# Performance work log

Hardware: AMD Instinct MI355X
Metric: run time of the kernel (lower is better)

Reference implementation:

```python
import jax, jax.numpy as jnp
import numpy as np

B, SQ, SK, D = 8, 4096, 4096, 64


def setup_inputs() -> dict:
    key = jax.random.key(0)
    k1, k2, k3 = jax.random.split(key, 3)
    x1 = jax.random.normal(k1, (B, SQ, D), dtype=jnp.float32)   # queries
    x2 = jax.random.normal(k2, (B, SK, D), dtype=jnp.float32)   # keys
    x3 = jax.random.normal(k3, (B, SK, D), dtype=jnp.float32)   # values
    x4 = 0                                                      # dropout p (static, 0 => deterministic)
    x5 = jnp.ones((1,), dtype=jnp.float32)                      # scale divisor
    return {"x1": x1, "x2": x2, "x3": x3, "x4": x4, "x5": x5}


def reference(x1, x2, x3, x4, x5):
    # scores: [B, Sq, Sk]
    scores = jnp.einsum("bqd,bkd->bqk", x1, x2) / x5
    attn = jax.nn.softmax(scores, axis=-1)
    p = float(x4)  # static python scalar
    if p > 0.0:
        mask = jax.random.bernoulli(jax.random.key(42), 1.0 - p, attn.shape)
        attn = attn * mask.astype(attn.dtype) / (1.0 - p)
    # out: [B, Sq, D]
    return jnp.einsum("bqk,bkd->bqd", attn, x3)
```

## Files before the change

kernel.cpp:

```cpp
#include <hip/hip_runtime.h>


typedef _Float16 f16x8 __attribute__((ext_vector_type(8)));
typedef _Float16 f16x4 __attribute__((ext_vector_type(4)));
typedef __fp16   h16x2 __attribute__((ext_vector_type(2)));
typedef float    f32x4 __attribute__((ext_vector_type(4)));

constexpr int kB  = 8;
constexpr int kSQ = 4096;
constexpr int kSK = 4096;
constexpr int kD  = 64;
constexpr int KSPLIT = 2;
constexpr int SKH = kSK / KSPLIT;
constexpr int BQ  = 128;
constexpr int BK  = 64;
constexpr int LDK = kD + 8;
constexpr int LDV = BK + 8;
constexpr int LDP = BK + 8;
constexpr size_t APART = (size_t)kB * kSQ * kD;

static __device__ __forceinline__ f16x4 pack4(float a, float b, float c, float d) {
    h16x2 p0 = __builtin_amdgcn_cvt_pkrtz(a, b);
    h16x2 p1 = __builtin_amdgcn_cvt_pkrtz(c, d);
    f16x4 r;
    r[0] = (_Float16)p0[0]; r[1] = (_Float16)p0[1];
    r[2] = (_Float16)p1[0]; r[3] = (_Float16)p1[1];
    return r;
}

__global__ __launch_bounds__(256, 2)
void fattn_partial(const float* __restrict__ Qg,
                   const float* __restrict__ Kg,
                   const float* __restrict__ Vg,
                   const float* __restrict__ sdiv,
                   float* __restrict__ Ap,
                   float2* __restrict__ MLp)
{
    __shared__ __align__(16) _Float16 sK[2][BK][LDK];
    __shared__ __align__(16) _Float16 sV[2][kD][LDV];
    __shared__ __align__(16) _Float16 sP[4][2][16][LDP];

    const int tid  = threadIdx.x;
    const int w    = tid >> 6;
    const int lane = tid & 63;
    const int l16  = lane & 15;
    const int quad = lane >> 4;

    const int b  = blockIdx.y;
    const int qb = blockIdx.x * BQ;
    const int ks = blockIdx.z;

    const float inv_scale = 1.0f / sdiv[0];

    const float* Qb = Qg + ((size_t)b * kSQ + qb) * kD;
    const float* Kb = Kg + ((size_t)b * kSK + (size_t)ks * SKH) * kD;
    const float* Vb = Vg + ((size_t)b * kSK + (size_t)ks * SKH) * kD;

    f16x8 qf[2][2];
#pragma unroll
    for (int mt = 0; mt < 2; ++mt) {
        const float* qrow = Qb + (size_t)(w * 32 + mt * 16 + l16) * kD;
#pragma unroll
        for (int kk = 0; kk < 2; ++kk) {
            const float4 a = *(const float4*)(qrow + kk * 32 + quad * 8);
            const float4 c = *(const float4*)(qrow + kk * 32 + quad * 8 + 4);
            f16x4 lo = pack4(a.x * inv_scale, a.y * inv_scale, a.z * inv_scale, a.w * inv_scale);
            f16x4 hi = pack4(c.x * inv_scale, c.y * inv_scale, c.z * inv_scale, c.w * inv_scale);
            f16x8 f;
            f[0] = lo[0]; f[1] = lo[1]; f[2] = lo[2]; f[3] = lo[3];
            f[4] = hi[0]; f[5] = hi[1]; f[6] = hi[2]; f[7] = hi[3];
            qf[mt][kk] = f;
        }
    }

    const int kp0 = 2 * ((0 * 256 + tid) >> 4), cb0 = ((0 * 256 + tid) & 15) * 4;
    const int kp1 = 2 * ((1 * 256 + tid) >> 4), cb1 = ((1 * 256 + tid) & 15) * 4;
    const int kq  = tid >> 4;
    const int fq  = tid & 15;
    const int kqs = (kq ^ (fq & 14)) * 4;

    float4 rk[2][2];
    float4 rv[4];

    auto load_tile = [&](int kt) {
        const float* Kt = Kb + (size_t)kt * BK * kD;
        const float* Vt = Vb + (size_t)kt * BK * kD;
        rk[0][0] = *(const float4*)(Kt + (kp0 + 0) * kD + cb0);
        rk[0][1] = *(const float4*)(Kt + (kp0 + 1) * kD + cb0);
        rk[1][0] = *(const float4*)(Kt + (kp1 + 0) * kD + cb1);
        rk[1][1] = *(const float4*)(Kt + (kp1 + 1) * kD + cb1);
#pragma unroll
        for (int r = 0; r < 4; ++r)
            rv[r] = *(const float4*)(Vt + (4 * kq + r) * kD + 4 * fq);
    };

    auto write_tile = [&](int buf) {
        *(f16x4*)&sK[buf][kp0 + 0][cb0] = pack4(rk[0][0].x, rk[0][0].y, rk[0][0].z, rk[0][0].w);
        *(f16x4*)&sK[buf][kp0 + 1][cb0] = pack4(rk[0][1].x, rk[0][1].y, rk[0][1].z, rk[0][1].w);
        *(f16x4*)&sK[buf][kp1 + 0][cb1] = pack4(rk[1][0].x, rk[1][0].y, rk[1][0].z, rk[1][0].w);
        *(f16x4*)&sK[buf][kp1 + 1][cb1] = pack4(rk[1][1].x, rk[1][1].y, rk[1][1].z, rk[1][1].w);
        const float vx[4][4] = {
            {rv[0].x, rv[0].y, rv[0].z, rv[0].w},
            {rv[1].x, rv[1].y, rv[1].z, rv[1].w},
            {rv[2].x, rv[2].y, rv[2].z, rv[2].w},
            {rv[3].x, rv[3].y, rv[3].z, rv[3].w}};
#pragma unroll
        for (int j = 0; j < 4; ++j)
            *(f16x4*)&sV[buf][4 * fq + j][kqs] =
                pack4(vx[0][j], vx[1][j], vx[2][j], vx[3][j]);
    };

    f32x4 o[2][4];
    float m_i[2] = {-1e30f, -1e30f}, l_i[2] = {0.0f, 0.0f};
#pragma unroll
    for (int mt = 0; mt < 2; ++mt)
#pragma unroll
        for (int dt = 0; dt < 4; ++dt)
#pragma unroll
            for (int r = 0; r < 4; ++r) o[mt][dt][r] = 0.0f;

    load_tile(0);
    write_tile(0);
    __syncthreads();

    const int nIter = SKH / BK;
    for (int kt = 0; kt < nIter; ++kt) {
        const int buf = kt & 1;
        const bool more = (kt + 1 < nIter);
        if (more) load_tile(kt + 1);

        f32x4 s[2][4];
#pragma unroll
        for (int nt = 0; nt < 4; ++nt) {
            const f16x8 kf0 = *(const f16x8*)&sK[buf][nt * 16 + l16][quad * 8];
            const f16x8 kf1 = *(const f16x8*)&sK[buf][nt * 16 + l16][32 + quad * 8];
#pragma unroll
            for (int mt = 0; mt < 2; ++mt) {
                f32x4 acc;
#pragma unroll
                for (int r = 0; r < 4; ++r) acc[r] = 0.0f;
                acc = __builtin_amdgcn_mfma_f32_16x16x32_f16(kf0, qf[mt][0], acc, 0, 0, 0);
                acc = __builtin_amdgcn_mfma_f32_16x16x32_f16(kf1, qf[mt][1], acc, 0, 0, 0);
                s[mt][nt] = acc;
            }
        }

#pragma unroll
        for (int mt = 0; mt < 2; ++mt) {
            float rm = s[mt][0][0];
#pragma unroll
            for (int nt = 0; nt < 4; ++nt)
#pragma unroll
                for (int r = 0; r < 4; ++r) rm = fmaxf(rm, s[mt][nt][r]);
            rm = fmaxf(rm, __shfl_xor(rm, 16, 64));
            rm = fmaxf(rm, __shfl_xor(rm, 32, 64));
            const float mnew = fmaxf(m_i[mt], rm);
            const float alpha = __expf(m_i[mt] - mnew);
            m_i[mt] = mnew;
            float rs = 0.0f;
#pragma unroll
            for (int nt = 0; nt < 4; ++nt)
#pragma unroll
                for (int r = 0; r < 4; ++r) {
                    const float p = __expf(s[mt][nt][r] - mnew);
                    s[mt][nt][r] = p;
                    rs += p;
                }
            rs += __shfl_xor(rs, 16, 64);
            rs += __shfl_xor(rs, 32, 64);
            l_i[mt] = l_i[mt] * alpha + rs;
#pragma unroll
            for (int dt = 0; dt < 4; ++dt)
#pragma unroll
                for (int r = 0; r < 4; ++r) o[mt][dt][r] *= alpha;
#pragma unroll
            for (int nt = 0; nt < 4; ++nt)
                *(f16x4*)&sP[w][mt][l16][nt * 16 + quad * 4] =
                    pack4(s[mt][nt][0], s[mt][nt][1], s[mt][nt][2], s[mt][nt][3]);
        }

        const f16x8 pfa0 = *(const f16x8*)&sP[w][0][l16][quad * 8];
        const f16x8 pfa1 = *(const f16x8*)&sP[w][0][l16][32 + quad * 8];
        const f16x8 pfb0 = *(const f16x8*)&sP[w][1][l16][quad * 8];
        const f16x8 pfb1 = *(const f16x8*)&sP[w][1][l16][32 + quad * 8];
#pragma unroll
        for (int dt = 0; dt < 4; ++dt) {
            const int f  = dt * 16 + l16;
            const int sw = (f >> 2) & 14;
            const f16x8 vf0 = *(const f16x8*)&sV[buf][f][((2 * quad) ^ sw) * 4];
            const f16x8 vf1 = *(const f16x8*)&sV[buf][f][((8 + 2 * quad) ^ sw) * 4];
            o[0][dt] = __builtin_amdgcn_mfma_f32_16x16x32_f16(vf0, pfa0, o[0][dt], 0, 0, 0);
            o[0][dt] = __builtin_amdgcn_mfma_f32_16x16x32_f16(vf1, pfa1, o[0][dt], 0, 0, 0);
            o[1][dt] = __builtin_amdgcn_mfma_f32_16x16x32_f16(vf0, pfb0, o[1][dt], 0, 0, 0);
            o[1][dt] = __builtin_amdgcn_mfma_f32_16x16x32_f16(vf1, pfb1, o[1][dt], 0, 0, 0);
        }

        if (more) write_tile(buf ^ 1);
        __syncthreads();
    }

    float* Ab = Ap + (size_t)ks * APART + ((size_t)b * kSQ + qb) * kD;
    float2* MLb = MLp + (size_t)ks * kB * kSQ + (size_t)b * kSQ + qb;
#pragma unroll
    for (int mt = 0; mt < 2; ++mt) {
        const int row = w * 32 + mt * 16 + l16;
#pragma unroll
        for (int dt = 0; dt < 4; ++dt) {
            float4 st4;
            st4.x = o[mt][dt][0];
            st4.y = o[mt][dt][1];
            st4.z = o[mt][dt][2];
            st4.w = o[mt][dt][3];
            *(float4*)&Ab[(size_t)row * kD + dt * 16 + quad * 4] = st4;
        }
        if (quad == 0) MLb[row] = make_float2(m_i[mt], l_i[mt]);
    }
}

__global__ __launch_bounds__(256)
void fattn_combine(const float* __restrict__ Ap,
                   const float2* __restrict__ MLp,
                   float* __restrict__ Og)
{
    const int idx = blockIdx.x * 256 + threadIdx.x;
    const int r = idx >> 4;
    const int c = (idx & 15) * 4;

    const float2 ml0 = MLp[r];
    const float2 ml1 = MLp[kB * kSQ + r];
    const float m = fmaxf(ml0.x, ml1.x);
    const float e0 = __expf(ml0.x - m);
    const float e1 = __expf(ml1.x - m);
    const float inv = 1.0f / (e0 * ml0.y + e1 * ml1.y);

    const float4 a0 = *(const float4*)&Ap[(size_t)r * kD + c];
    const float4 a1 = *(const float4*)&Ap[APART + (size_t)r * kD + c];
    float4 res;
    res.x = (e0 * a0.x + e1 * a1.x) * inv;
    res.y = (e0 * a0.y + e1 * a1.y) * inv;
    res.z = (e0 * a0.z + e1 * a1.z) * inv;
    res.w = (e0 * a0.w + e1 * a1.w) * inv;
    *(float4*)&Og[(size_t)r * kD + c] = res;
}

extern "C" void kernel_launch(void* const* d_in, const int* in_sizes, int n_in,
                              void* d_out, int out_size, void* d_ws, size_t ws_size,
                              hipStream_t stream) {
    const float* Q    = (const float*)d_in[0];
    const float* K    = (const float*)d_in[1];
    const float* V    = (const float*)d_in[2];
    const float* sdiv = (const float*)d_in[4];
    float* O = (float*)d_out;

    float*  Ap  = (float*)d_ws;
    float2* MLp = (float2*)(Ap + KSPLIT * APART);

    dim3 grid(kSQ / BQ, kB, KSPLIT);
    fattn_partial<<<grid, dim3(256), 0, stream>>>(Q, K, V, sdiv, Ap, MLp);
    fattn_combine<<<dim3(kB * kSQ * kD / (256 * 4)), dim3(256), 0, stream>>>(Ap, MLp, O);
}
```

Measured before the change: 153.9 us.

## Pre-convert K/V to swizzled fp16 and stream tiles directly into LDS

After: 146.7 us. 1.05x faster.

```diff
diff --git a/kernel.cpp b/kernel.cpp
--- a/kernel.cpp
+++ b/kernel.cpp
@@ -10,12 +10,10 @@
 constexpr int kSQ = 4096;
 constexpr int kSK = 4096;
 constexpr int kD  = 64;
-constexpr int KSPLIT = 2;
+constexpr int KSPLIT = 4;
 constexpr int SKH = kSK / KSPLIT;
 constexpr int BQ  = 128;
 constexpr int BK  = 64;
-constexpr int LDK = kD + 8;
-constexpr int LDV = BK + 8;
 constexpr int LDP = BK + 8;
 constexpr size_t APART = (size_t)kB * kSQ * kD;
 
@@ -27,17 +25,84 @@
     r[2] = (_Float16)p1[0]; r[3] = (_Float16)p1[1];
     return r;
 }
+static __device__ __forceinline__ f16x8 pack8(const float4& a, const float4& c) {
+    f16x4 lo = pack4(a.x, a.y, a.z, a.w);
+    f16x4 hi = pack4(c.x, c.y, c.z, c.w);
+    f16x8 f;
+    f[0] = lo[0]; f[1] = lo[1]; f[2] = lo[2]; f[3] = lo[3];
+    f[4] = hi[0]; f[5] = hi[1]; f[6] = hi[2]; f[7] = hi[3];
+    return f;
+}
+
+typedef const __attribute__((address_space(1))) unsigned int* gu32p;
+typedef __attribute__((address_space(3))) unsigned int* lu32p;
+static __device__ __forceinline__ void gload_lds16(const void* g, void* l) {
+    __builtin_amdgcn_global_load_lds((gu32p)g, (lu32p)l, 16, 0, 0);
+}
 
 __global__ __launch_bounds__(256, 2)
+void fattn_prepass(const float* __restrict__ Kg,
+                   const float* __restrict__ Vg,
+                   _Float16* __restrict__ Kh,
+                   _Float16* __restrict__ Vt)
+{
+    __shared__ _Float16 tr[kD][BK];
+
+    const int tid = threadIdx.x;
+    const int kt  = blockIdx.x;
+    const int b   = blockIdx.y;
+
+    const int k = tid >> 2;
+    const int p = tid & 3;
+    const int gk = kt * BK + k;
+
+    {
+        const float* src = Kg + ((size_t)b * kSK + gk) * kD + p * 16;
+        const float4 a0 = *(const float4*)(src + 0);
+        const float4 a1 = *(const float4*)(src + 4);
+        const float4 a2 = *(const float4*)(src + 8);
+        const float4 a3 = *(const float4*)(src + 12);
+        _Float16* dst = Kh + ((size_t)b * kSK + gk) * kD;
+        const int fb0 = 2 * p, fb1 = 2 * p + 1;
+        *(f16x8*)&dst[(fb0 ^ (gk & 7)) * 8] = pack8(a0, a1);
+        *(f16x8*)&dst[(fb1 ^ (gk & 7)) * 8] = pack8(a2, a3);
+    }
+
+    {
+        const float* src = Vg + ((size_t)b * kSK + gk) * kD + p * 16;
+        const float4 a0 = *(const float4*)(src + 0);
+        const float4 a1 = *(const float4*)(src + 4);
+        const float4 a2 = *(const float4*)(src + 8);
+        const float4 a3 = *(const float4*)(src + 12);
+        const float v[16] = {a0.x,a0.y,a0.z,a0.w, a1.x,a1.y,a1.z,a1.w,
+                             a2.x,a2.y,a2.z,a2.w, a3.x,a3.y,a3.z,a3.w};
+#pragma unroll
+        for (int j = 0; j < 16; ++j)
+            tr[p * 16 + j][k] = (_Float16)v[j];
+    }
+    __syncthreads();
+    {
+        const int f  = tid >> 2;
+        const int p2 = tid & 3;
+        const f16x8 b0 = *(const f16x8*)&tr[f][p2 * 16 + 0];
+        const f16x8 b1 = *(const f16x8*)&tr[f][p2 * 16 + 8];
+        _Float16* dst = Vt + (((size_t)b * 64 + kt) * kD + f) * BK;
+        const int kb0 = 2 * p2, kb1 = 2 * p2 + 1;
+        *(f16x8*)&dst[(kb0 ^ (f & 7)) * 8] = b0;
+        *(f16x8*)&dst[(kb1 ^ (f & 7)) * 8] = b1;
+    }
+}
+
+__global__ __launch_bounds__(256, 3)
 void fattn_partial(const float* __restrict__ Qg,
-                   const float* __restrict__ Kg,
-                   const float* __restrict__ Vg,
+                   const _Float16* __restrict__ Kh,
+                   const _Float16* __restrict__ Vt,
                    const float* __restrict__ sdiv,
-                   float* __restrict__ Ap,
+                   _Float16* __restrict__ Ap,
                    float2* __restrict__ MLp)
 {
-    __shared__ __align__(16) _Float16 sK[2][BK][LDK];
-    __shared__ __align__(16) _Float16 sV[2][kD][LDV];
+    __shared__ __align__(16) _Float16 sK[2][BK * kD];
+    __shared__ __align__(16) _Float16 sV[2][kD * BK];
     __shared__ __align__(16) _Float16 sP[4][2][16][LDP];
 
     const int tid  = threadIdx.x;
@@ -45,6 +110,7 @@
     const int lane = tid & 63;
     const int l16  = lane & 15;
     const int quad = lane >> 4;
+    const int sw   = (quad ^ (l16 & 7)) * 8;
 
     const int b  = blockIdx.y;
     const int qb = blockIdx.x * BQ;
@@ -53,8 +119,8 @@
     const float inv_scale = 1.0f / sdiv[0];
 
     const float* Qb = Qg + ((size_t)b * kSQ + qb) * kD;
-    const float* Kb = Kg + ((size_t)b * kSK + (size_t)ks * SKH) * kD;
-    const float* Vb = Vg + ((size_t)b * kSK + (size_t)ks * SKH) * kD;
+    const _Float16* Khb = Kh + ((size_t)b * kSK + (size_t)ks * SKH) * kD;
+    const _Float16* Vtb = Vt + (((size_t)b * 64 + (size_t)ks * (SKH / BK)) * kD) * BK;
 
     f16x8 qf[2][2];
 #pragma unroll
@@ -64,50 +130,21 @@
         for (int kk = 0; kk < 2; ++kk) {
             const float4 a = *(const float4*)(qrow + kk * 32 + quad * 8);
             const float4 c = *(const float4*)(qrow + kk * 32 + quad * 8 + 4);
-            f16x4 lo = pack4(a.x * inv_scale, a.y * inv_scale, a.z * inv_scale, a.w * inv_scale);
-            f16x4 hi = pack4(c.x * inv_scale, c.y * inv_scale, c.z * inv_scale, c.w * inv_scale);
-            f16x8 f;
-            f[0] = lo[0]; f[1] = lo[1]; f[2] = lo[2]; f[3] = lo[3];
-            f[4] = hi[0]; f[5] = hi[1]; f[6] = hi[2]; f[7] = hi[3];
-            qf[mt][kk] = f;
-        }
-    }
-
-    const int kp0 = 2 * ((0 * 256 + tid) >> 4), cb0 = ((0 * 256 + tid) & 15) * 4;
-    const int kp1 = 2 * ((1 * 256 + tid) >> 4), cb1 = ((1 * 256 + tid) & 15) * 4;
-    const int kq  = tid >> 4;
-    const int fq  = tid & 15;
-    const int kqs = (kq ^ (fq & 14)) * 4;
-
-    float4 rk[2][2];
-    float4 rv[4];
-
-    auto load_tile = [&](int kt) {
-        const float* Kt = Kb + (size_t)kt * BK * kD;
-        const float* Vt = Vb + (size_t)kt * BK * kD;
-        rk[0][0] = *(const float4*)(Kt + (kp0 + 0) * kD + cb0);
-        rk[0][1] = *(const float4*)(Kt + (kp0 + 1) * kD + cb0);
-        rk[1][0] = *(const float4*)(Kt + (kp1 + 0) * kD + cb1);
-        rk[1][1] = *(const float4*)(Kt + (kp1 + 1) * kD + cb1);
-#pragma unroll
-        for (int r = 0; r < 4; ++r)
-            rv[r] = *(const float4*)(Vt + (4 * kq + r) * kD + 4 * fq);
-    };
-
-    auto write_tile = [&](int buf) {
-        *(f16x4*)&sK[buf][kp0 + 0][cb0] = pack4(rk[0][0].x, rk[0][0].y, rk[0][0].z, rk[0][0].w);
-        *(f16x4*)&sK[buf][kp0 + 1][cb0] = pack4(rk[0][1].x, rk[0][1].y, rk[0][1].z, rk[0][1].w);
-        *(f16x4*)&sK[buf][kp1 + 0][cb1] = pack4(rk[1][0].x, rk[1][0].y, rk[1][0].z, rk[1][0].w);
-        *(f16x4*)&sK[buf][kp1 + 1][cb1] = pack4(rk[1][1].x, rk[1][1].y, rk[1][1].z, rk[1][1].w);
-        const float vx[4][4] = {
-            {rv[0].x, rv[0].y, rv[0].z, rv[0].w},
-            {rv[1].x, rv[1].y, rv[1].z, rv[1].w},
-            {rv[2].x, rv[2].y, rv[2].z, rv[2].w},
-            {rv[3].x, rv[3].y, rv[3].z, rv[3].w}};
-#pragma unroll
-        for (int j = 0; j < 4; ++j)
-            *(f16x4*)&sV[buf][4 * fq + j][kqs] =
-                pack4(vx[0][j], vx[1][j], vx[2][j], vx[3][j]);
+            float4 as = make_float4(a.x * inv_scale, a.y * inv_scale, a.z * inv_scale, a.w * inv_scale);
+            float4 cs = make_float4(c.x * inv_scale, c.y * inv_scale, c.z * inv_scale, c.w * inv_scale);
+            qf[mt][kk] = pack8(as, cs);
+        }
+    }
+
+    auto stage = [&](int kt, int buf) {
+        const char* gk = (const char*)(Khb + (size_t)kt * BK * kD) + w * 2048 + lane * 16;
+        const char* gv = (const char*)(Vtb + (size_t)kt * kD * BK) + w * 2048 + lane * 16;
+        char* lk = (char*)&sK[buf][0] + w * 2048;
+        char* lv = (char*)&sV[buf][0] + w * 2048;
+        gload_lds16(gk,        lk);
+        gload_lds16(gk + 1024, lk + 1024);
+        gload_lds16(gv,        lv);
+        gload_lds16(gv + 1024, lv + 1024);
     };
 
     f32x4 o[2][4];
@@ -119,21 +156,21 @@
 #pragma unroll
             for (int r = 0; r < 4; ++r) o[mt][dt][r] = 0.0f;
 
-    load_tile(0);
-    write_tile(0);
+    stage(0, 0);
     __syncthreads();
 
     const int nIter = SKH / BK;
     for (int kt = 0; kt < nIter; ++kt) {
         const int buf = kt & 1;
         const bool more = (kt + 1 < nIter);
-        if (more) load_tile(kt + 1);
+        if (more) stage(kt + 1, buf ^ 1);
 
         f32x4 s[2][4];
 #pragma unroll
         for (int nt = 0; nt < 4; ++nt) {
-            const f16x8 kf0 = *(const f16x8*)&sK[buf][nt * 16 + l16][quad * 8];
-            const f16x8 kf1 = *(const f16x8*)&sK[buf][nt * 16 + l16][32 + quad * 8];
+            const int krow = (nt * 16 + l16) * kD;
+            const f16x8 kf0 = *(const f16x8*)&sK[buf][krow + sw];
+            const f16x8 kf1 = *(const f16x8*)&sK[buf][krow + (sw ^ 32)];
 #pragma unroll
             for (int mt = 0; mt < 2; ++mt) {
                 f32x4 acc;
@@ -185,40 +222,33 @@
         const f16x8 pfb1 = *(const f16x8*)&sP[w][1][l16][32 + quad * 8];
 #pragma unroll
         for (int dt = 0; dt < 4; ++dt) {
-            const int f  = dt * 16 + l16;
-            const int sw = (f >> 2) & 14;
-            const f16x8 vf0 = *(const f16x8*)&sV[buf][f][((2 * quad) ^ sw) * 4];
-            const f16x8 vf1 = *(const f16x8*)&sV[buf][f][((8 + 2 * quad) ^ sw) * 4];
+            const int frow = (dt * 16 + l16) * BK;
+            const f16x8 vf0 = *(const f16x8*)&sV[buf][frow + sw];
+            const f16x8 vf1 = *(const f16x8*)&sV[buf][frow + (sw ^ 32)];
             o[0][dt] = __builtin_amdgcn_mfma_f32_16x16x32_f16(vf0, pfa0, o[0][dt], 0, 0, 0);
             o[0][dt] = __builtin_amdgcn_mfma_f32_16x16x32_f16(vf1, pfa1, o[0][dt], 0, 0, 0);
             o[1][dt] = __builtin_amdgcn_mfma_f32_16x16x32_f16(vf0, pfb0, o[1][dt], 0, 0, 0);
             o[1][dt] = __builtin_amdgcn_mfma_f32_16x16x32_f16(vf1, pfb1, o[1][dt], 0, 0, 0);
         }
 
-        if (more) write_tile(buf ^ 1);
         __syncthreads();
     }
 
-    float* Ab = Ap + (size_t)ks * APART + ((size_t)b * kSQ + qb) * kD;
+    _Float16* Ab = Ap + (size_t)ks * APART + ((size_t)b * kSQ + qb) * kD;
     float2* MLb = MLp + (size_t)ks * kB * kSQ + (size_t)b * kSQ + qb;
 #pragma unroll
     for (int mt = 0; mt < 2; ++mt) {
         const int row = w * 32 + mt * 16 + l16;
 #pragma unroll
-        for (int dt = 0; dt < 4; ++dt) {
-            float4 st4;
-            st4.x = o[mt][dt][0];
-            st4.y = o[mt][dt][1];
-            st4.z = o[mt][dt][2];
-            st4.w = o[mt][dt][3];
-            *(float4*)&Ab[(size_t)row * kD + dt * 16 + quad * 4] = st4;
-        }
+        for (int dt = 0; dt < 4; ++dt)
+            *(f16x4*)&Ab[(size_t)row * kD + dt * 16 + quad * 4] =
+                pack4(o[mt][dt][0], o[mt][dt][1], o[mt][dt][2], o[mt][dt][3]);
         if (quad == 0) MLb[row] = make_float2(m_i[mt], l_i[mt]);
     }
 }
 
 __global__ __launch_bounds__(256)
-void fattn_combine(const float* __restrict__ Ap,
+void fattn_combine(const _Float16* __restrict__ Ap,
                    const float2* __restrict__ MLp,
                    float* __restrict__ Og)
 {
@@ -226,20 +256,25 @@
     const int r = idx >> 4;
     const int c = (idx & 15) * 4;
 
-    const float2 ml0 = MLp[r];
-    const float2 ml1 = MLp[kB * kSQ + r];
-    const float m = fmaxf(ml0.x, ml1.x);
-    const float e0 = __expf(ml0.x - m);
-    const float e1 = __expf(ml1.x - m);
-    const float inv = 1.0f / (e0 * ml0.y + e1 * ml1.y);
-
-    const float4 a0 = *(const float4*)&Ap[(size_t)r * kD + c];
-    const float4 a1 = *(const float4*)&Ap[APART + (size_t)r * kD + c];
-    float4 res;
-    res.x = (e0 * a0.x + e1 * a1.x) * inv;
-    res.y = (e0 * a0.y + e1 * a1.y) * inv;
-    res.z = (e0 * a0.z + e1 * a1.z) * inv;
-    res.w = (e0 * a0.w + e1 * a1.w) * inv;
+    float m = -1e30f;
+    float2 ml[KSPLIT];
+#pragma unroll
+    for (int s = 0; s < KSPLIT; ++s) {
+        ml[s] = MLp[(size_t)s * kB * kSQ + r];
+        m = fmaxf(m, ml[s].x);
+    }
+    float acc[4] = {0.f, 0.f, 0.f, 0.f};
+    float lsum = 0.f;
+#pragma unroll
+    for (int s = 0; s < KSPLIT; ++s) {
+        const float e = __expf(ml[s].x - m);
+        lsum += e * ml[s].y;
+        const f16x4 a = *(const f16x4*)&Ap[(size_t)s * APART + (size_t)r * kD + c];
+#pragma unroll
+        for (int j = 0; j < 4; ++j) acc[j] += e * (float)a[j];
+    }
+    const float inv = 1.0f / lsum;
+    float4 res = make_float4(acc[0] * inv, acc[1] * inv, acc[2] * inv, acc[3] * inv);
     *(float4*)&Og[(size_t)r * kD + c] = res;
 }
 
@@ -252,10 +287,13 @@
     const float* sdiv = (const float*)d_in[4];
     float* O = (float*)d_out;
 
-    float*  Ap  = (float*)d_ws;
-    float2* MLp = (float2*)(Ap + KSPLIT * APART);
-
+    _Float16* Kh  = (_Float16*)d_ws;
+    _Float16* Vt  = Kh + (size_t)kB * kSK * kD;
+    _Float16* Ap  = Vt + (size_t)kB * kSK * kD;
+    float2*   MLp = (float2*)(Ap + (size_t)KSPLIT * APART);
+
+    fattn_prepass<<<dim3(kSK / BK, kB), dim3(256), 0, stream>>>(K, V, Kh, Vt);
     dim3 grid(kSQ / BQ, kB, KSPLIT);
-    fattn_partial<<<grid, dim3(256), 0, stream>>>(Q, K, V, sdiv, Ap, MLp);
+    fattn_partial<<<grid, dim3(256), 0, stream>>>(Q, Kh, Vt, sdiv, Ap, MLp);
     fattn_combine<<<dim3(kB * kSQ * kD / (256 * 4)), dim3(256), 0, stream>>>(Ap, MLp, O);
 }
```
